# Optimization experiments

Hardware: AMD Instinct MI355X
Metric: run time of the kernel (lower is better)

Reference implementation:

```python
import jax, jax.numpy as jnp
import numpy as np

NR = 100000   # router nodes
NP = 200000   # packet nodes
H = 128       # h_dim
E_PASS = 600000   # router -> router
E_CONN = 600000   # packet -> router
E_TRANS = 600000  # router -> packet


def setup_inputs() -> dict:
    key = jax.random.key(0)
    ks = jax.random.split(key, 12)
    return {
        "router_feat": jax.random.normal(ks[0], (NR, H), jnp.float32),
        "packet_feat": jax.random.normal(ks[1], (NP, H), jnp.float32),
        "W_r": jax.random.normal(ks[2], (2 * H, H), jnp.float32) * 0.05,
        "b_r": jax.random.normal(ks[3], (H,), jnp.float32) * 0.05,
        "W_p": jax.random.normal(ks[4], (H, H), jnp.float32) * 0.05,
        "b_p": jax.random.normal(ks[5], (H,), jnp.float32) * 0.05,
        "pass_src": jax.random.randint(ks[6], (E_PASS,), 0, NR, jnp.int32),
        "pass_dst": jax.random.randint(ks[7], (E_PASS,), 0, NR, jnp.int32),
        "connect_src": jax.random.randint(ks[8], (E_CONN,), 0, NP, jnp.int32),
        "connect_dst": jax.random.randint(ks[9], (E_CONN,), 0, NR, jnp.int32),
        "transfer_src": jax.random.randint(ks[10], (E_TRANS,), 0, NR, jnp.int32),
        "transfer_dst": jax.random.randint(ks[11], (E_TRANS,), 0, NP, jnp.int32),
    }


def reference(router_feat, packet_feat, W_r, b_r, W_p, b_p,
              pass_src, pass_dst, connect_src, connect_dst,
              transfer_src, transfer_dst):
    # relation 'pass': router -> router, copy_u + sum -> h1 (router)
    h1_r = jax.ops.segment_sum(router_feat[pass_src], pass_dst, num_segments=NR)
    # relation 'connect': packet -> router, copy_u + sum -> h2 (router)
    h2_r = jax.ops.segment_sum(packet_feat[connect_src], connect_dst, num_segments=NR)
    # relation 'transfer': router -> packet, copy_u + mean -> h1 (packet)
    s = jax.ops.segment_sum(router_feat[transfer_src], transfer_dst, num_segments=NP)
    cnt = jax.ops.segment_sum(jnp.ones((E_TRANS,), jnp.float32), transfer_dst,
                              num_segments=NP)
    # DGL mean: zero for zero in-degree nodes
    h1_p = s / jnp.maximum(cnt, 1.0)[:, None]

    # router update: feat += ReLU(Linear(concat([h1, h2])))
    router_out = router_feat + jax.nn.relu(
        jnp.concatenate([h1_r, h2_r], axis=-1) @ W_r + b_r)
    # packet update: feat += ReLU(Linear(h1))
    packet_out = packet_feat + jax.nn.relu(h1_p @ W_p + b_p)
    return router_out, packet_out
```

## Files before the change

kernel.cpp:

```cpp
#include <hip/hip_runtime.h>

#define H_DIM 128

typedef __attribute__((ext_vector_type(8))) short short8v;
typedef __attribute__((ext_vector_type(4))) float f32x4;

__device__ __forceinline__ ushort f2bf(float f) {
  unsigned u = __builtin_bit_cast(unsigned, f);
  u += 0x7fffu + ((u >> 16) & 1u);
  return (ushort)(u >> 16);
}
__device__ __forceinline__ float bflo(unsigned u) {
  return __builtin_bit_cast(float, u << 16);
}
__device__ __forceinline__ float bfhi(unsigned u) {
  return __builtin_bit_cast(float, u & 0xffff0000u);
}

__global__ __launch_bounds__(256) void histcast_k(
    const float* __restrict__ W_r, const float* __restrict__ W_p,
    ushort* __restrict__ Wt, const int* __restrict__ d0,
    const int* __restrict__ d1, const int* __restrict__ d2,
    int* __restrict__ ro, int n0, int n1, int n2, int NRn) {
  int bid = blockIdx.x;
  if (bid < 192) {
    int i = bid * 256 + threadIdx.x;
    int m = i >> 14;
    int j = (i >> 7) & 127;
    int k = i & 127;
    float v = (m == 0)   ? W_r[k * 128 + j]
              : (m == 1) ? W_r[(128 + k) * 128 + j]
                         : W_p[k * 128 + j];
    Wt[i] = f2bf(v);
  } else {
    int e = (bid - 192) * 256 + threadIdx.x;
    if (e < n0)
      atomicAdd(&ro[d0[e]], 1);
    else if (e < n0 + n1)
      atomicAdd(&ro[NRn + d1[e - n0]], 1);
    else if (e < n0 + n1 + n2)
      atomicAdd(&ro[2 * NRn + d2[e - n0 - n1]], 1);
  }
}

__global__ __launch_bounds__(256) void scan1_k(int* __restrict__ a, int n,
                                               int* __restrict__ bsums) {
  __shared__ int ts[256];
  int t = threadIdx.x;
  int base = blockIdx.x * 2048 + t * 8;
  int v[8];
  int s = 0;
#pragma unroll
  for (int k = 0; k < 8; ++k) {
    v[k] = (base + k < n) ? a[base + k] : 0;
    s += v[k];
  }
  ts[t] = s;
  __syncthreads();
  for (int off = 1; off < 256; off <<= 1) {
    int x = (t >= off) ? ts[t - off] : 0;
    __syncthreads();
    ts[t] += x;
    __syncthreads();
  }
  if (t == 0) bsums[blockIdx.x] = ts[255];
  int run = (t == 0) ? 0 : ts[t - 1];
#pragma unroll
  for (int k = 0; k < 8; ++k) {
    int x = v[k];
    if (base + k < n) a[base + k] = run;
    run += x;
  }
}

__global__ __launch_bounds__(256) void scan2_k(int* __restrict__ bsums,
                                               int nb) {
  __shared__ int ts[256];
  int t = threadIdx.x;
  int v = (t < nb) ? bsums[t] : 0;
  ts[t] = v;
  __syncthreads();
  for (int off = 1; off < 256; off <<= 1) {
    int x = (t >= off) ? ts[t - off] : 0;
    __syncthreads();
    ts[t] += x;
    __syncthreads();
  }
  int excl = (t == 0) ? 0 : ts[t - 1];
  if (t < nb) bsums[t] = excl;
}

__global__ __launch_bounds__(256) void scan3_k(int* __restrict__ a, int n,
                                               const int* __restrict__ bsums,
                                               int total) {
  int i = blockIdx.x * blockDim.x + threadIdx.x;
  if (i < n) a[i] += bsums[i / 2048];
  if (i == 0) a[n] = total;
}

__global__ __launch_bounds__(256) void permgemm_k(
    const float* __restrict__ rf, const float* __restrict__ pf,
    const ushort* __restrict__ Wt, ushort* __restrict__ Y1,
    ushort* __restrict__ Y2, ushort* __restrict__ Yp,
    const int* __restrict__ s0a, const int* __restrict__ d0a,
    const int* __restrict__ s1a, const int* __restrict__ d1a,
    const int* __restrict__ s2a, const int* __restrict__ d2a,
    const int* __restrict__ ro, int* __restrict__ cnt2, int* __restrict__ es,
    int nb1, int nb2, int M1, int M2, int n0, int n1, int n2, int NRn, int ng,
    int np) {
  __shared__ float lds_f[8192];
  int bid = blockIdx.x;
  int nmin = ng < np ? ng : np;
  bool do_gemm;
  int idx;
  if (bid < 2 * nmin) {
    do_gemm = !(bid & 1);
    idx = bid >> 1;
  } else {
    idx = nmin + (bid - 2 * nmin);
    do_gemm = ng > np;
  }

  if (!do_gemm) {
    long e = (long)idx * 256 + threadIdx.x;
    int src, slot;
    if (e < n0) {
      slot = d0a[e];
      src = s0a[e];
    } else if (e < n0 + n1) {
      long i = e - n0;
      slot = NRn + d1a[i];
      src = s1a[i];
    } else if (e < n0 + n1 + n2) {
      long i = e - n0 - n1;
      slot = 2 * NRn + d2a[i];
      src = s2a[i];
    } else
      return;
    int p = ro[slot] + atomicAdd(&cnt2[slot], 1);
    es[p] = src;
    return;
  }

  ushort* wl = (ushort*)lds_f;
  const float* X;
  ushort* Y;
  const ushort* Wg;
  int M, row0;
  if (idx < nb1) {
    X = rf; Y = Y1; Wg = Wt; M = M1; row0 = idx * 64;
  } else if (idx < nb1 + nb2) {
    X = pf; Y = Y2; Wg = Wt + 16384; M = M2; row0 = (idx - nb1) * 64;
  } else {
    X = rf; Y = Yp; Wg = Wt + 32768; M = M1; row0 = (idx - nb1 - nb2) * 64;
  }

  int tid = threadIdx.x;
  {
    const uint4* src = (const uint4*)Wg;
    for (int i = tid; i < 2048; i += 256) {
      int j = i >> 4;
      int k8 = (i & 15) * 8;
      int kk = k8 ^ ((j & 7) << 3);
      *(uint4*)&wl[j * 128 + kk] = src[i];
    }
  }
  __syncthreads();

  int lane = tid & 63;
  int wv = tid >> 6;
  int l15 = lane & 15;
  int kq = lane >> 4;
  int rowl = wv * 16 + l15;
  int grow = row0 + rowl;
  int growc = grow < M ? grow : M - 1;

  f32x4 acc[8];
#pragma unroll
  for (int t = 0; t < 8; ++t) {
    f32x4 z = {0.f, 0.f, 0.f, 0.f};
    acc[t] = z;
  }

#pragma unroll
  for (int ks = 0; ks < 4; ++ks) {
    int k0 = ks * 32;
    const float* ap = X + (long)growc * H_DIM + k0 + kq * 8;
    float4 a0 = *(const float4*)ap;
    float4 a1 = *(const float4*)(ap + 4);
    short8v af;
    af[0] = (short)f2bf(a0.x);
    af[1] = (short)f2bf(a0.y);
    af[2] = (short)f2bf(a0.z);
    af[3] = (short)f2bf(a0.w);
    af[4] = (short)f2bf(a1.x);
    af[5] = (short)f2bf(a1.y);
    af[6] = (short)f2bf(a1.z);
    af[7] = (short)f2bf(a1.w);
#pragma unroll
    for (int nt = 0; nt < 8; ++nt) {
      int j = nt * 16 + l15;
      int kk = (k0 + kq * 8) ^ ((j & 7) << 3);
      short8v bf = *(const short8v*)&wl[j * 128 + kk];
      acc[nt] =
          __builtin_amdgcn_mfma_f32_16x16x32_bf16(af, bf, acc[nt], 0, 0, 0);
    }
  }
  __syncthreads();
#pragma unroll
  for (int nt = 0; nt < 8; ++nt) {
#pragma unroll
    for (int r = 0; r < 4; ++r) {
      int rl = wv * 16 + kq * 4 + r;
      int col = nt * 16 + l15;
      lds_f[rl * 128 + col] = acc[nt][r];
    }
  }
  __syncthreads();
  for (int i = tid; i < 2048; i += 256) {
    float4 v = *(const float4*)&lds_f[i * 4];
    int flat = i * 4;
    int r = flat >> 7;
    int cc = flat & 127;
    int gr = row0 + r;
    if (gr < M) {
      ushort4 o;
      o.x = f2bf(v.x);
      o.y = f2bf(v.y);
      o.z = f2bf(v.z);
      o.w = f2bf(v.w);
      *(ushort4*)&Y[(long)gr * H_DIM + cc] = o;
    }
  }
}

__device__ __forceinline__ void gacc16(const ushort* __restrict__ Y,
                                       const int* __restrict__ es, int e0,
                                       int e1, int c8, float* a) {
  int e = e0;
  for (; e + 3 < e1; e += 4) {
    uint4 v0 = *(const uint4*)(Y + (long)es[e] * H_DIM + c8);
    uint4 v1 = *(const uint4*)(Y + (long)es[e + 1] * H_DIM + c8);
    uint4 v2 = *(const uint4*)(Y + (long)es[e + 2] * H_DIM + c8);
    uint4 v3 = *(const uint4*)(Y + (long)es[e + 3] * H_DIM + c8);
    a[0] += (bflo(v0.x) + bflo(v1.x)) + (bflo(v2.x) + bflo(v3.x));
    a[1] += (bfhi(v0.x) + bfhi(v1.x)) + (bfhi(v2.x) + bfhi(v3.x));
    a[2] += (bflo(v0.y) + bflo(v1.y)) + (bflo(v2.y) + bflo(v3.y));
    a[3] += (bfhi(v0.y) + bfhi(v1.y)) + (bfhi(v2.y) + bfhi(v3.y));
    a[4] += (bflo(v0.z) + bflo(v1.z)) + (bflo(v2.z) + bflo(v3.z));
    a[5] += (bfhi(v0.z) + bfhi(v1.z)) + (bfhi(v2.z) + bfhi(v3.z));
    a[6] += (bflo(v0.w) + bflo(v1.w)) + (bflo(v2.w) + bflo(v3.w));
    a[7] += (bfhi(v0.w) + bfhi(v1.w)) + (bfhi(v2.w) + bfhi(v3.w));
  }
  for (; e < e1; ++e) {
    uint4 v = *(const uint4*)(Y + (long)es[e] * H_DIM + c8);
    a[0] += bflo(v.x);
    a[1] += bfhi(v.x);
    a[2] += bflo(v.y);
    a[3] += bfhi(v.y);
    a[4] += bflo(v.z);
    a[5] += bfhi(v.z);
    a[6] += bflo(v.w);
    a[7] += bfhi(v.w);
  }
}

__global__ __launch_bounds__(256) void gather_k(
    const ushort* __restrict__ Y1, const ushort* __restrict__ Y2,
    const ushort* __restrict__ Yp, const int* __restrict__ ro,
    const int* __restrict__ es, const float* __restrict__ rf,
    const float* __restrict__ pf, const float* __restrict__ b_r,
    const float* __restrict__ b_p, float* __restrict__ out_r,
    float* __restrict__ out_p, int nrb, int NRn, int NPn) {
  int tid = threadIdx.x;
  int lane = tid & 63;
  int wv = tid >> 6;
  int sub = lane >> 4;
  int c8 = (lane & 15) * 8;
  int bid = blockIdx.x;

  float a[8] = {0.f, 0.f, 0.f, 0.f, 0.f, 0.f, 0.f, 0.f};
  if (bid < nrb) {
    int row = bid * 16 + wv * 4 + sub;
    if (row >= NRn) return;
    gacc16(Y1, es, ro[row], ro[row + 1], c8, a);
    gacc16(Y2, es, ro[NRn + row], ro[NRn + row + 1], c8, a);
    float4 bb0 = *(const float4*)&b_r[c8];
    float4 bb1 = *(const float4*)&b_r[c8 + 4];
    float bv[8] = {bb0.x, bb0.y, bb0.z, bb0.w, bb1.x, bb1.y, bb1.z, bb1.w};
    const f32x4* rp = (const f32x4*)&rf[(long)row * H_DIM + c8];
    f32x4 rv0 = __builtin_nontemporal_load(rp);
    f32x4 rv1 = __builtin_nontemporal_load(rp + 1);
    f32x4 o0, o1;
#pragma unroll
    for (int i = 0; i < 4; ++i) {
      float v = a[i] + bv[i];
      v = v > 0.f ? v : 0.f;
      o0[i] = rv0[i] + v;
      float v2 = a[i + 4] + bv[i + 4];
      v2 = v2 > 0.f ? v2 : 0.f;
      o1[i] = rv1[i] + v2;
    }
    f32x4* op = (f32x4*)&out_r[(long)row * H_DIM + c8];
    __builtin_nontemporal_store(o0, op);
    __builtin_nontemporal_store(o1, op + 1);
  } else {
    int row = (bid - nrb) * 16 + wv * 4 + sub;
    if (row >= NPn) return;
    int e0 = ro[2 * NRn + row], e1 = ro[2 * NRn + row + 1];
    gacc16(Yp, es, e0, e1, c8, a);
    int deg = e1 - e0;
    float inv = 1.0f / (float)(deg > 1 ? deg : 1);
    float4 bb0 = *(const float4*)&b_p[c8];
    float4 bb1 = *(const float4*)&b_p[c8 + 4];
    float bv[8] = {bb0.x, bb0.y, bb0.z, bb0.w, bb1.x, bb1.y, bb1.z, bb1.w};
    const f32x4* pp = (const f32x4*)&pf[(long)row * H_DIM + c8];
    f32x4 pv0 = __builtin_nontemporal_load(pp);
    f32x4 pv1 = __builtin_nontemporal_load(pp + 1);
    f32x4 o0, o1;
#pragma unroll
    for (int i = 0; i < 4; ++i) {
      float v = a[i] * inv + bv[i];
      v = v > 0.f ? v : 0.f;
      o0[i] = pv0[i] + v;
      float v2 = a[i + 4] * inv + bv[i + 4];
      v2 = v2 > 0.f ? v2 : 0.f;
      o1[i] = pv1[i] + v2;
    }
    f32x4* op = (f32x4*)&out_p[(long)row * H_DIM + c8];
    __builtin_nontemporal_store(o0, op);
    __builtin_nontemporal_store(o1, op + 1);
  }
}

extern "C" void kernel_launch(void* const* d_in, const int* in_sizes, int n_in,
                              void* d_out, int out_size, void* d_ws,
                              size_t ws_size, hipStream_t stream) {
  const float* router_feat = (const float*)d_in[0];
  const float* packet_feat = (const float*)d_in[1];
  const float* W_r = (const float*)d_in[2];
  const float* b_r = (const float*)d_in[3];
  const float* W_p = (const float*)d_in[4];
  const float* b_p = (const float*)d_in[5];
  const int* pass_src = (const int*)d_in[6];
  const int* pass_dst = (const int*)d_in[7];
  const int* connect_src = (const int*)d_in[8];
  const int* connect_dst = (const int*)d_in[9];
  const int* transfer_src = (const int*)d_in[10];
  const int* transfer_dst = (const int*)d_in[11];

  const int NRn = in_sizes[0] / H_DIM;
  const int NPn = in_sizes[1] / H_DIM;
  const int E0 = in_sizes[6], E1 = in_sizes[8], E2 = in_sizes[10];
  const long Etot = (long)E0 + E1 + E2;
  const int nseg = 2 * NRn + NPn;

  float* out_r = (float*)d_out;
  float* out_p = out_r + (size_t)NRn * H_DIM;

  int* ro = (int*)d_ws;
  int* cnt2 = ro + (nseg + 1);
  int* es = cnt2 + nseg;
  int* bsums = es + Etot;
  size_t int_count = (size_t)(nseg + 1) + nseg + Etot + 256;
  size_t byte_off = ((int_count * 4) + 15) & ~(size_t)15;
  ushort* Y1 = (ushort*)((char*)d_ws + byte_off);
  ushort* Y2 = Y1 + (size_t)NRn * H_DIM;
  ushort* Yp = Y2 + (size_t)NPn * H_DIM;
  ushort* Wt = Yp + (size_t)NRn * H_DIM;

  (void)hipMemsetAsync(ro, 0, (size_t)(2 * nseg + 1) * sizeof(int), stream);

  int egrid = (int)((Etot + 255) / 256);
  histcast_k<<<192 + egrid, 256, 0, stream>>>(W_r, W_p, Wt, pass_dst,
                                              connect_dst, transfer_dst, ro, E0,
                                              E1, E2, NRn);
  int nb = (nseg + 2047) / 2048;
  scan1_k<<<nb, 256, 0, stream>>>(ro, nseg, bsums);
  scan2_k<<<1, 256, 0, stream>>>(bsums, nb);
  scan3_k<<<(nseg + 255) / 256, 256, 0, stream>>>(ro, nseg, bsums, (int)Etot);

  int nb1 = (NRn + 63) / 64, nb2 = (NPn + 63) / 64, nb3 = nb1;
  int ng = nb1 + nb2 + nb3;
  int np = egrid;
  permgemm_k<<<ng + np, 256, 0, stream>>>(
      router_feat, packet_feat, Wt, Y1, Y2, Yp, pass_src, pass_dst, connect_src,
      connect_dst, transfer_src, transfer_dst, ro, cnt2, es, nb1, nb2, NRn, NPn,
      E0, E1, E2, NRn, ng, np);

  int nrb = (NRn + 15) / 16, npb = (NPn + 15) / 16;
  gather_k<<<nrb + npb, 256, 0, stream>>>(Y1, Y2, Yp, ro, es, router_feat,
                                          packet_feat, b_r, b_p, out_r, out_p,
                                          nrb, NRn, NPn);
}
```

Baseline: 358.1 us.

## Record histogram atomic ranks, fuse scan passes, interleave blocks, swizzle LDS epilogue

```diff
diff --git a/kernel.cpp b/kernel.cpp
--- a/kernel.cpp
+++ b/kernel.cpp
@@ -21,7 +21,8 @@
     const float* __restrict__ W_r, const float* __restrict__ W_p,
     ushort* __restrict__ Wt, const int* __restrict__ d0,
     const int* __restrict__ d1, const int* __restrict__ d2,
-    int* __restrict__ ro, int n0, int n1, int n2, int NRn) {
+    int* __restrict__ ro, int* __restrict__ rank, int n0, int n1, int n2,
+    int NRn) {
   int bid = blockIdx.x;
   if (bid < 192) {
     int i = bid * 256 + threadIdx.x;
@@ -34,12 +35,16 @@
     Wt[i] = f2bf(v);
   } else {
     int e = (bid - 192) * 256 + threadIdx.x;
+    int slot;
     if (e < n0)
-      atomicAdd(&ro[d0[e]], 1);
+      slot = d0[e];
     else if (e < n0 + n1)
-      atomicAdd(&ro[NRn + d1[e - n0]], 1);
+      slot = NRn + d1[e - n0];
     else if (e < n0 + n1 + n2)
-      atomicAdd(&ro[2 * NRn + d2[e - n0 - n1]], 1);
+      slot = 2 * NRn + d2[e - n0 - n1];
+    else
+      return;
+    rank[e] = atomicAdd(&ro[slot], 1);
   }
 }
 
@@ -73,8 +78,9 @@
   }
 }
 
-__global__ __launch_bounds__(256) void scan2_k(int* __restrict__ bsums,
-                                               int nb) {
+__global__ __launch_bounds__(256) void scan23_k(int* __restrict__ a, int n,
+                                                const int* __restrict__ bsums,
+                                                int nb, int total) {
   __shared__ int ts[256];
   int t = threadIdx.x;
   int v = (t < nb) ? bsums[t] : 0;
@@ -86,16 +92,15 @@
     ts[t] += x;
     __syncthreads();
   }
-  int excl = (t == 0) ? 0 : ts[t - 1];
-  if (t < nb) bsums[t] = excl;
-}
-
-__global__ __launch_bounds__(256) void scan3_k(int* __restrict__ a, int n,
-                                               const int* __restrict__ bsums,
-                                               int total) {
-  int i = blockIdx.x * blockDim.x + threadIdx.x;
-  if (i < n) a[i] += bsums[i / 2048];
-  if (i == 0) a[n] = total;
+  int b = blockIdx.x;
+  int excl = (b == 0) ? 0 : ts[b - 1];
+  int base = b * 2048;
+#pragma unroll
+  for (int k = 0; k < 8; ++k) {
+    int i = base + k * 256 + t;
+    if (i < n) a[i] += excl;
+  }
+  if (b == 0 && t == 0) a[n] = total;
 }
 
 __global__ __launch_bounds__(256) void permgemm_k(
@@ -105,21 +110,16 @@
     const int* __restrict__ s0a, const int* __restrict__ d0a,
     const int* __restrict__ s1a, const int* __restrict__ d1a,
     const int* __restrict__ s2a, const int* __restrict__ d2a,
-    const int* __restrict__ ro, int* __restrict__ cnt2, int* __restrict__ es,
-    int nb1, int nb2, int M1, int M2, int n0, int n1, int n2, int NRn, int ng,
-    int np) {
+    const int* __restrict__ ro, const int* __restrict__ rank,
+    int* __restrict__ es, int nb1, int nb2, int M1, int M2, int n0, int n1,
+    int n2, int NRn, int ng, int np) {
   __shared__ float lds_f[8192];
-  int bid = blockIdx.x;
-  int nmin = ng < np ? ng : np;
-  bool do_gemm;
-  int idx;
-  if (bid < 2 * nmin) {
-    do_gemm = !(bid & 1);
-    idx = bid >> 1;
-  } else {
-    idx = nmin + (bid - 2 * nmin);
-    do_gemm = ng > np;
-  }
+  long T = (long)ng + np;
+  long b = blockIdx.x;
+  int g_before = (int)((b * ng) / T);
+  int g_incl = (int)(((b + 1) * ng) / T);
+  bool do_gemm = g_incl > g_before;
+  int idx = do_gemm ? g_before : (int)(b - g_before);
 
   if (!do_gemm) {
     long e = (long)idx * 256 + threadIdx.x;
@@ -137,8 +137,7 @@
       src = s2a[i];
     } else
       return;
-    int p = ro[slot] + atomicAdd(&cnt2[slot], 1);
-    es[p] = src;
+    es[ro[slot] + rank[e]] = src;
     return;
   }
 
@@ -212,16 +211,17 @@
 #pragma unroll
     for (int r = 0; r < 4; ++r) {
       int rl = wv * 16 + kq * 4 + r;
-      int col = nt * 16 + l15;
+      int col = (nt * 16 + l15) ^ (kq << 4);
       lds_f[rl * 128 + col] = acc[nt][r];
     }
   }
   __syncthreads();
   for (int i = tid; i < 2048; i += 256) {
-    float4 v = *(const float4*)&lds_f[i * 4];
     int flat = i * 4;
     int r = flat >> 7;
     int cc = flat & 127;
+    int sw = ((r >> 2) & 3) << 4;
+    float4 v = *(const float4*)&lds_f[r * 128 + (cc ^ sw)];
     int gr = row0 + r;
     if (gr < M) {
       ushort4 o;
@@ -359,33 +359,32 @@
   float* out_p = out_r + (size_t)NRn * H_DIM;
 
   int* ro = (int*)d_ws;
-  int* cnt2 = ro + (nseg + 1);
-  int* es = cnt2 + nseg;
+  int* rank = ro + (nseg + 1);
+  int* es = rank + Etot;
   int* bsums = es + Etot;
-  size_t int_count = (size_t)(nseg + 1) + nseg + Etot + 256;
+  size_t int_count = (size_t)(nseg + 1) + 2 * (size_t)Etot + 256;
   size_t byte_off = ((int_count * 4) + 15) & ~(size_t)15;
   ushort* Y1 = (ushort*)((char*)d_ws + byte_off);
   ushort* Y2 = Y1 + (size_t)NRn * H_DIM;
   ushort* Yp = Y2 + (size_t)NPn * H_DIM;
   ushort* Wt = Yp + (size_t)NRn * H_DIM;
 
-  (void)hipMemsetAsync(ro, 0, (size_t)(2 * nseg + 1) * sizeof(int), stream);
+  (void)hipMemsetAsync(ro, 0, (size_t)(nseg + 1) * sizeof(int), stream);
 
   int egrid = (int)((Etot + 255) / 256);
   histcast_k<<<192 + egrid, 256, 0, stream>>>(W_r, W_p, Wt, pass_dst,
-                                              connect_dst, transfer_dst, ro, E0,
-                                              E1, E2, NRn);
+                                              connect_dst, transfer_dst, ro,
+                                              rank, E0, E1, E2, NRn);
   int nb = (nseg + 2047) / 2048;
   scan1_k<<<nb, 256, 0, stream>>>(ro, nseg, bsums);
-  scan2_k<<<1, 256, 0, stream>>>(bsums, nb);
-  scan3_k<<<(nseg + 255) / 256, 256, 0, stream>>>(ro, nseg, bsums, (int)Etot);
+  scan23_k<<<nb, 256, 0, stream>>>(ro, nseg, bsums, nb, (int)Etot);
 
   int nb1 = (NRn + 63) / 64, nb2 = (NPn + 63) / 64, nb3 = nb1;
   int ng = nb1 + nb2 + nb3;
   int np = egrid;
   permgemm_k<<<ng + np, 256, 0, stream>>>(
       router_feat, packet_feat, Wt, Y1, Y2, Yp, pass_src, pass_dst, connect_src,
-      connect_dst, transfer_src, transfer_dst, ro, cnt2, es, nb1, nb2, NRn, NPn,
+      connect_dst, transfer_src, transfer_dst, ro, rank, es, nb1, nb2, NRn, NPn,
       E0, E1, E2, NRn, ng, np);
 
   int nrb = (NRn + 15) / 16, npb = (NPn + 15) / 16;
```

After: 321.0 us. -10.3%, faster.
